# Optimization experiments

Measured on AMD Instinct MI355X. Metric: run time of the kernel, lower is better.

The kernel has to match this reference:

```python
import jax, jax.numpy as jnp
import numpy as np

T_TOK, N_UNITS, E, H, L_PATH, N_PATHS, B, VOCAB = 16, 4096, 128, 128, 32, 1024, 8, 16384
MAX_PATH_LEN = 32
PAD_ID = 0


def _run_lstm(x, Wi, Wh, b):
    # x: [T, N, E]; torch gate order i, f, g, o
    Hh = Wh.shape[1]
    h0 = jnp.zeros((x.shape[1], Hh), x.dtype)
    def step(carry, xt):
        h, c = carry
        g = xt @ Wi.T + h @ Wh.T + b
        i, f, gg, o = jnp.split(g, 4, axis=-1)
        c = jax.nn.sigmoid(f) * c + jax.nn.sigmoid(i) * jnp.tanh(gg)
        h = jax.nn.sigmoid(o) * jnp.tanh(c)
        return (h, c), h
    _, ys = jax.lax.scan(step, (h0, h0), x)
    return ys


def _bilstm(x, lengths, Wif, Whf, bf, Wib, Whb, bb):
    # emulates pack_padded_sequence + bidirectional LSTM + pad_packed (zeros past length)
    T = x.shape[0]
    t = jnp.arange(T)[:, None]
    valid = t < lengths[None, :]
    out_f = _run_lstm(x, Wif, Whf, bf)
    rev = jnp.clip(lengths[None, :] - 1 - t, 0, T - 1)  # reverse within each valid prefix
    x_rev = jnp.take_along_axis(x, rev[:, :, None], axis=0)
    out_b = jnp.take_along_axis(_run_lstm(x_rev, Wib, Whb, bb), rev[:, :, None], axis=0)
    return jnp.concatenate([out_f, out_b], axis=-1) * valid[:, :, None]


def _layernorm(x, g, b):
    m = x.mean(-1, keepdims=True)
    v = ((x - m) ** 2).mean(-1, keepdims=True)
    return (x - m) * jax.lax.rsqrt(v + 1e-5) * g + b


def _forward(units, paths, unit_per_data, path_per_data, emb, tl_Wif, tl_Whf, tl_bf,
             tl_Wib, tl_Whb, tl_bb, lin_W, lin_b, ln_g, ln_b, attn_w, attn_b,
             pl_Wif, pl_Whf, pl_bf, pl_Wib, pl_Whb, pl_bb, ul_W, ul_b):
    # ---- _token_encoder ----
    is_pad = units == PAD_ID
    tok_len = jnp.where(is_pad.any(0), jnp.argmax(is_pad, 0), units.shape[0])
    x = emb[units]                                              # [T, NU, E]
    h = _bilstm(x, tok_len, tl_Wif, tl_Whf, tl_bf, tl_Wib, tl_Whb, tl_bb)  # [T, NU, 2H]
    out = h @ lin_W.T + lin_b                                   # [T, NU, E]
    q = jnp.tanh(_layernorm(out, ln_g, ln_b))
    scores = q @ attn_w.T + attn_b                              # [T, NU, 1] local attention
    scores = jnp.where(is_pad[:, :, None], -1e9, scores)
    w = jax.nn.softmax(scores, axis=0)
    tok_feat = jnp.einsum('tn,tne->ne', w[..., 0], out)         # [NU, E]
    # ---- _unit_to_path (vectorized ragged gather) ----
    Lp, Pn = paths.shape
    has_end = (paths == -1).any(0)
    fe = jnp.where(has_end, jnp.argmax(paths == -1, 0), Lp)
    ML = min(Lp, MAX_PATH_LEN)
    nb = unit_per_data.shape[0]
    data_of_path = jnp.repeat(jnp.arange(nb), path_per_data, total_repeat_length=Pn)
    u_off = jnp.cumsum(unit_per_data) - unit_per_data
    off_p = u_off[data_of_path]
    un_p = unit_per_data[data_of_path]
    pL = paths[:ML]
    t = jnp.arange(ML)[:, None]
    within = t < fe[None, :]
    keep = within & (pL >= 0) & (pL < un_p[None, :])
    gidx = jnp.clip(jnp.clip(pL, 0, None) + off_p[None, :], 0, tok_feat.shape[0] - 1)
    feats = tok_feat[gidx] * keep[:, :, None]                   # [ML, P, E]
    mask = jnp.where(within, (pL < 0) | (pL > un_p[None, :]), True)
    # ---- _path_encoder ----
    p_len = jnp.where(mask.any(0), jnp.argmax(mask, 0), ML)
    hp = _bilstm(feats, p_len, pl_Wif, pl_Whf, pl_bf, pl_Wib, pl_Whb, pl_bb)
    return hp @ ul_W.T + ul_b                                   # [ML, P, E]


def setup_inputs() -> dict:
    rng = np.random.default_rng(0)
    tok_len = rng.integers(4, T_TOK + 1, N_UNITS); tok_len[0] = T_TOK
    units = rng.integers(1, VOCAB, (T_TOK, N_UNITS))
    units = np.where(np.arange(T_TOK)[:, None] < tok_len[None, :], units, PAD_ID)
    upd = N_UNITS // B
    p_len = rng.integers(8, L_PATH + 1, N_PATHS); p_len[0] = L_PATH
    paths = rng.integers(0, upd, (L_PATH, N_PATHS))
    paths = np.where(np.arange(L_PATH)[:, None] < p_len[None, :], paths, -1)
    key = jax.random.key(0)
    ks = iter(jax.random.split(key, 24))
    def pn(shape, s=0.08):
        return (jax.random.normal(next(ks), shape) * s).astype(jnp.float32)
    return dict(
        units=jnp.asarray(units, jnp.int32),
        paths=jnp.asarray(paths, jnp.int32),
        unit_per_data=jnp.full((B,), upd, jnp.int32),
        path_per_data=jnp.full((B,), N_PATHS // B, jnp.int32),
        emb=pn((VOCAB, E)),
        tl_Wif=pn((4 * H, E)), tl_Whf=pn((4 * H, H)), tl_bf=pn((4 * H,)),
        tl_Wib=pn((4 * H, E)), tl_Whb=pn((4 * H, H)), tl_bb=pn((4 * H,)),
        lin_W=pn((E, 2 * H)), lin_b=pn((E,)),
        ln_g=jnp.ones((E,), jnp.float32), ln_b=jnp.zeros((E,), jnp.float32),
        attn_w=pn((1, E)), attn_b=pn((1,)),
        pl_Wif=pn((4 * H, E)), pl_Whf=pn((4 * H, H)), pl_bf=pn((4 * H,)),
        pl_Wib=pn((4 * H, E)), pl_Whb=pn((4 * H, H)), pl_bb=pn((4 * H,)),
        ul_W=pn((E, 2 * H)), ul_b=pn((E,)),
    )


def reference(units, paths, unit_per_data, path_per_data, emb, tl_Wif, tl_Whf, tl_bf,
              tl_Wib, tl_Whb, tl_bb, lin_W, lin_b, ln_g, ln_b, attn_w, attn_b,
              pl_Wif, pl_Whf, pl_bf, pl_Wib, pl_Whb, pl_bb, ul_W, ul_b):
    return _forward(units, paths, unit_per_data, path_per_data, emb, tl_Wif, tl_Whf, tl_bf,
                    tl_Wib, tl_Whb, tl_bb, lin_W, lin_b, ln_g, ln_b, attn_w, attn_b,
                    pl_Wif, pl_Whf, pl_bf, pl_Wib, pl_Whb, pl_bb, ul_W, ul_b)
```

## Files before the change

### kernel.cpp

```cpp
#include <hip/hip_runtime.h>
#include <cstdint>
#include <cstddef>

#define T_TOKN 16
#define NUNITS 4096
#define LPATH  32
#define NPATHS 1024
#define BNUM   8

typedef __attribute__((ext_vector_type(8))) short short8;
typedef __attribute__((ext_vector_type(4))) short short4x;
typedef __attribute__((ext_vector_type(4))) float f32x4;

enum : size_t {
  OFF_WFRAG   = 0,
  OFF_LINFRAG = 262144,
  OFF_OUTF    = 294912,
  OFF_OUTB    = OFF_OUTF + 4194304,
  OFF_OUTLIN  = OFF_OUTB + 4194304,
  OFF_SCORES  = OFF_OUTLIN + 8388608,
  OFF_TOKFEAT = OFF_SCORES + 65536,
  OFF_POUTF   = OFF_TOKFEAT + 524288,
  OFF_POUTB   = OFF_POUTF + 2097152,
  OFF_INT     = OFF_POUTB + 2097152,
  WS_FLOATS   = OFF_INT + 8192
};

static __device__ __forceinline__ unsigned short f2bf(float f) {
  union { float f; unsigned u; } v; v.f = f;
  unsigned r = v.u + 0x7fffu + ((v.u >> 16) & 1u);
  return (unsigned short)(r >> 16);
}
static __device__ __forceinline__ float bf2f(unsigned short u) {
  union { unsigned u; float f; } v; v.u = ((unsigned)u) << 16;
  return v.f;
}
static __device__ __forceinline__ unsigned pack_bf(float a, float b) {
  return (unsigned)f2bf(a) | ((unsigned)f2bf(b) << 16);
}
static __device__ __forceinline__ float sigf(float x)      { return 1.f / (1.f + __expf(-x)); }
static __device__ __forceinline__ float tanhfast(float x)  { return 2.f / (1.f + __expf(-2.f * x)) - 1.f; }

__global__ void prep_kernel(
    const float* __restrict__ tWif, const float* __restrict__ tWhf,
    const float* __restrict__ tWib, const float* __restrict__ tWhb,
    const float* __restrict__ pWif, const float* __restrict__ pWhf,
    const float* __restrict__ pWib, const float* __restrict__ pWhb,
    const float* __restrict__ linW, const float* __restrict__ ulW,
    const int* __restrict__ units, const int* __restrict__ paths,
    const int* __restrict__ upd, const int* __restrict__ ppd,
    float* __restrict__ ws, int* __restrict__ ip)
{
  int idx = blockIdx.x * 256 + threadIdx.x;
  if (idx < 524288) {
    unsigned short* wf = (unsigned short*)(ws + OFF_WFRAG);
    int mat = idx >> 17, rem = idx & 131071;
    int i  = rem & 7;
    int lane = (rem >> 3) & 63;
    int ct = (rem >> 9) & 3;
    int ks = (rem >> 11) & 7;
    int wv = (rem >> 14) & 7;
    int g = wv * 64 + ct * 16 + (lane & 15);
    int k = ks * 32 + ((lane >> 4) << 3) + i;
    const float* Wi; const float* Wh;
    switch (mat) {
      case 0: Wi = tWif; Wh = tWhf; break;
      case 1: Wi = tWib; Wh = tWhb; break;
      case 2: Wi = pWif; Wh = pWhf; break;
      default: Wi = pWib; Wh = pWhb; break;
    }
    float v = (k < 128) ? Wi[g * 128 + k] : Wh[g * 128 + (k - 128)];
    wf[idx] = f2bf(v);
  } else if (idx < 524288 + 65536) {
    unsigned short* lf = (unsigned short*)(ws + OFF_LINFRAG);
    int i2 = idx - 524288;
    int mat = i2 >> 15, rem = i2 & 32767;
    int i  = rem & 7;
    int lane = (rem >> 3) & 63;
    int ks = (rem >> 9) & 7;
    int ct = (rem >> 12) & 7;
    int e = ct * 16 + (lane & 15);
    int k = ks * 32 + ((lane >> 4) << 3) + i;
    const float* W = mat ? ulW : linW;
    lf[i2] = f2bf(W[e * 256 + k]);
  } else if (idx < 589824 + 4096) {
    int n = idx - 589824;
    int len = T_TOKN;
    for (int t = 0; t < T_TOKN; ++t)
      if (units[t * NUNITS + n] == 0) { len = t; break; }
    ip[n] = len;
  } else if (idx < 589824 + 5120) {
    int p = idx - (589824 + 4096);
    int* fe_a  = ip + 4096;
    int* p_len = ip + 5120;
    int* off_p = ip + 6144;
    int* un_p  = ip + 7168;
    int cum = 0; int d = BNUM - 1;
    for (int dd = 0; dd < BNUM; ++dd) {
      int c2 = cum + ppd[dd];
      if (p < c2) { d = dd; break; }
      cum = c2;
    }
    int off = 0;
    for (int dd = 0; dd < d; ++dd) off += upd[dd];
    int un = upd[d];
    off_p[p] = off; un_p[p] = un;
    int f = LPATH;
    for (int t = 0; t < LPATH; ++t)
      if (paths[t * NPATHS + p] == -1) { f = t; break; }
    fe_a[p] = f;
    int pl = LPATH;
    for (int t = 0; t < LPATH; ++t) {
      int v = paths[t * NPATHS + p];
      if ((t >= f) || (v < 0) || (v > un)) { pl = t; break; }
    }
    p_len[p] = pl;
  }
}

template <int MODE>
__global__ __launch_bounds__(1024, 4) void lstm_kernel(
    const unsigned short* __restrict__ wfragAll,
    const float* __restrict__ biasF, const float* __restrict__ biasB,
    const float* __restrict__ src,
    const int* __restrict__ idxsrc,
    const int* __restrict__ lens,
    const int* __restrict__ fe_a, const int* __restrict__ off_p, const int* __restrict__ un_p,
    unsigned short* __restrict__ outF, unsigned short* __restrict__ outB)
{
  constexpr int NN   = MODE ? NPATHS : NUNITS;
  constexpr int TT   = MODE ? LPATH : T_TOKN;
  constexpr int M    = MODE ? 8 : 32;
  constexpr int MR   = MODE ? 16 : 32;
  constexpr int NRT  = MR / 16;
  constexpr int ASTR = 264;
  constexpr int GSTR = 514;

  __shared__ unsigned short ash[MR * ASTR];
  __shared__ float gates[MR * GSTR];
  __shared__ int   idxL[M * TT];

  int tid  = threadIdx.x;
  int dir  = blockIdx.y;
  int n0   = blockIdx.x * M;
  int lane = tid & 63, wv = tid >> 6;

  const unsigned short* wbase =
      wfragAll + (size_t)((MODE ? 2 : 0) + dir) * 131072;
  int wv8 = wv >> 1;
  short8 bfr[8][2];
#pragma unroll
  for (int ks = 0; ks < 8; ++ks)
#pragma unroll
    for (int c2 = 0; c2 < 2; ++c2) {
      int ct = ((wv & 1) << 1) | c2;
      bfr[ks][c2] = *(const short8*)&wbase[((((wv8 * 8 + ks) * 4 + ct) * 64) + lane) * 8];
    }

  if (MODE == 0) {
    for (int i = tid; i < MR * 128; i += 1024)
      ash[(i >> 7) * ASTR + 128 + (i & 127)] = 0;
  } else {
    for (int i = tid; i < MR * ASTR; i += 1024) ash[i] = 0;
  }
  for (int i = tid; i < M * TT; i += 1024) {
    int u = i / TT, tt = i - u * TT;
    idxL[i] = idxsrc[tt * NN + (n0 + u)];
  }

  const float* bcp = dir ? biasB : biasF;
  int j2 = MODE ? (tid & 127) : ((tid & 63) * 2);
  int ug = MODE ? (tid >> 7)  : (tid >> 6);
  float2 b2[4];
#pragma unroll
  for (int q = 0; q < 4; ++q) {
    if (MODE == 0) b2[q] = *(const float2*)&bcp[q * 128 + j2];
    else           b2[q] = make_float2(bcp[q * 128 + j2], 0.f);
  }
  constexpr int NU = MODE ? 1 : 2;
  float cst0[NU], cst1[NU];
  int   ulen[NU];
#pragma unroll
  for (int i = 0; i < NU; ++i) {
    cst0[i] = 0.f; cst1[i] = 0.f;
    ulen[i] = lens[n0 + ug * NU + i];
  }

  int gu, gk0;
  if (MODE == 0) { gu = tid >> 5; gk0 = (tid & 31) * 4; }
  else           { gu = tid >> 7; gk0 = tid & 127; }
  int gn = n0 + gu;
  int glen = lens[gn];
  int gfe = 0, goff = 0, gun = 0;
  if (MODE) { gfe = fe_a[gn]; goff = off_p[gn]; gun = un_p[gn]; }

  float4 xq; float xs;
  __syncthreads();

  {
    int tau = dir ? min(max(glen - 1, 0), TT - 1) : 0;
    int v = idxL[gu * TT + tau];
    if (MODE == 0) {
      xq = *(const float4*)&src[(size_t)v * 128 + gk0];
    } else {
      bool keep = (tau < gfe) && (v >= 0) && (v < gun);
      xs = keep ? src[(size_t)min(v + goff, NUNITS - 1) * 128 + gk0] : 0.f;
    }
  }
  if (MODE == 0) {
    short4x x4;
    x4[0] = (short)f2bf(xq.x); x4[1] = (short)f2bf(xq.y);
    x4[2] = (short)f2bf(xq.z); x4[3] = (short)f2bf(xq.w);
    *(short4x*)&ash[gu * ASTR + gk0] = x4;
  } else {
    ash[gu * ASTR + gk0] = f2bf(xs);
  }
  __syncthreads();

#pragma unroll 1
  for (int t = 0; t < TT; ++t) {
    {
      int tn = (t + 1 < TT) ? t + 1 : t;
      int taun = dir ? min(max(glen - 1 - tn, 0), TT - 1) : tn;
      int vn = idxL[gu * TT + taun];
      f32x4 acc[NRT][2];
#pragma unroll
      for (int rt = 0; rt < NRT; ++rt)
#pragma unroll
        for (int c2 = 0; c2 < 2; ++c2) {
          f32x4 z = {0.f, 0.f, 0.f, 0.f};
          acc[rt][c2] = z;
        }
#pragma unroll
      for (int ks = 0; ks < 8; ++ks) {
        short8 afr[NRT];
#pragma unroll
        for (int rt = 0; rt < NRT; ++rt)
          afr[rt] = *(const short8*)&ash[(rt * 16 + (lane & 15)) * ASTR + ks * 32 + ((lane >> 4) << 3)];
#pragma unroll
        for (int rt = 0; rt < NRT; ++rt)
#pragma unroll
          for (int c2 = 0; c2 < 2; ++c2)
            acc[rt][c2] = __builtin_amdgcn_mfma_f32_16x16x32_bf16(
                afr[rt], bfr[ks][c2], acc[rt][c2], 0, 0, 0);
      }
      if (MODE == 0) {
        xq = *(const float4*)&src[(size_t)vn * 128 + gk0];
      } else {
        bool keep = (taun < gfe) && (vn >= 0) && (vn < gun);
        xs = keep ? src[(size_t)min(vn + goff, NUNITS - 1) * 128 + gk0] : 0.f;
      }
#pragma unroll
      for (int rt = 0; rt < NRT; ++rt)
#pragma unroll
        for (int c2 = 0; c2 < 2; ++c2) {
          int g = wv * 32 + c2 * 16 + (lane & 15);
#pragma unroll
          for (int r = 0; r < 4; ++r) {
            int u = rt * 16 + ((lane >> 4) << 2) + r;
            gates[u * GSTR + g] = acc[rt][c2][r];
          }
        }
    }
    __syncthreads();

#pragma unroll
    for (int i = 0; i < NU; ++i) {
      int u = ug * NU + i;
      int n = n0 + u;
      int L = ulen[i];
      if (t < L) {
        if (MODE == 0) {
          float2 g0 = *(const float2*)&gates[u * GSTR + j2];
          float2 g1 = *(const float2*)&gates[u * GSTR + 128 + j2];
          float2 g2 = *(const float2*)&gates[u * GSTR + 256 + j2];
          float2 g3 = *(const float2*)&gates[u * GSTR + 384 + j2];
          float i0 = sigf(g0.x + b2[0].x), i1 = sigf(g0.y + b2[0].y);
          float f0 = sigf(g1.x + b2[1].x), f1 = sigf(g1.y + b2[1].y);
          float c0 = tanhfast(g2.x + b2[2].x), c1 = tanhfast(g2.y + b2[2].y);
          float o0 = sigf(g3.x + b2[3].x), o1 = sigf(g3.y + b2[3].y);
          float cA = f0 * cst0[i] + i0 * c0;
          float cB = f1 * cst1[i] + i1 * c1;
          cst0[i] = cA; cst1[i] = cB;
          unsigned hp = pack_bf(o0 * tanhfast(cA), o1 * tanhfast(cB));
          *(unsigned*)&ash[u * ASTR + 128 + j2] = hp;
          if (dir == 0) {
            *(unsigned*)&outF[((size_t)t * NN + n) * 128 + j2] = hp;
          } else {
            *(unsigned*)&outB[((size_t)(L - 1 - t) * NN + n) * 128 + j2] = hp;
          }
        } else {
          float p0 = gates[u * GSTR + j2]       + b2[0].x;
          float p1 = gates[u * GSTR + 128 + j2] + b2[1].x;
          float p2 = gates[u * GSTR + 256 + j2] + b2[2].x;
          float p3 = gates[u * GSTR + 384 + j2] + b2[3].x;
          float ig = sigf(p0), fg = sigf(p1), gg = tanhfast(p2), og = sigf(p3);
          float c = fg * cst0[i] + ig * gg;
          cst0[i] = c;
          unsigned short hb = f2bf(og * tanhfast(c));
          ash[u * ASTR + 128 + j2] = hb;
          if (dir == 0) outF[((size_t)t * NN + n) * 128 + j2] = hb;
          else          outB[((size_t)(L - 1 - t) * NN + n) * 128 + j2] = hb;
        }
      } else {
        if (MODE == 0) {
          if (dir == 0) *(unsigned*)&outF[((size_t)t * NN + n) * 128 + j2] = 0u;
          else          *(unsigned*)&outB[((size_t)t * NN + n) * 128 + j2] = 0u;
        } else {
          if (dir == 0) outF[((size_t)t * NN + n) * 128 + j2] = 0;
          else          outB[((size_t)t * NN + n) * 128 + j2] = 0;
        }
      }
    }
    if (t + 1 < TT) {
      if (MODE == 0) {
        short4x x4;
        x4[0] = (short)f2bf(xq.x); x4[1] = (short)f2bf(xq.y);
        x4[2] = (short)f2bf(xq.z); x4[3] = (short)f2bf(xq.w);
        *(short4x*)&ash[gu * ASTR + gk0] = x4;
      } else {
        ash[gu * ASTR + gk0] = f2bf(xs);
      }
    }
    __syncthreads();
  }
}

template <int EPI>
__global__ __launch_bounds__(256) void gemm_mfma(
    const unsigned short* __restrict__ INf, const unsigned short* __restrict__ INb,
    const int* __restrict__ lens,
    const unsigned short* __restrict__ Bfrag, const float* __restrict__ bias,
    void* __restrict__ OUTv, float* __restrict__ scores,
    const float* __restrict__ lng, const float* __restrict__ lnb,
    const float* __restrict__ attw, const float* __restrict__ attb,
    const int* __restrict__ units, int Nn)
{
  constexpr int OSTR = 132;
  __shared__ float outs[64 * OSTR];
  __shared__ float red1[256];
  __shared__ float red2[256];
  __shared__ float rowm[64], rowr[64];
  __shared__ float awsh[128], lgsh[128], lbsh[128];

  int tid = threadIdx.x, lane = tid & 63, wv = tid >> 6;
  int row0 = blockIdx.x * 64;
  int t = row0 / Nn, n0 = row0 % Nn;

  if (EPI == 1 && tid < 128) {
    awsh[tid] = attw[tid]; lgsh[tid] = lng[tid]; lbsh[tid] = lnb[tid];
  }

  short8 bfr[8][2];
#pragma unroll
  for (int ks = 0; ks < 8; ++ks)
#pragma unroll
    for (int c2 = 0; c2 < 2; ++c2) {
      int ct = wv * 2 + c2;
      bfr[ks][c2] = *(const short8*)&Bfrag[(((ct * 8 + ks) * 64) + lane) * 8];
    }

  int rb = lane & 15;
  int koq = (lane >> 4) << 3;
  bool val[4];
#pragma unroll
  for (int rt = 0; rt < 4; ++rt)
    val[rt] = (EPI == 1) ? true : (t < lens[n0 + rt * 16 + rb]);

  f32x4 acc[4][2];
#pragma unroll
  for (int rt = 0; rt < 4; ++rt)
#pragma unroll
    for (int c2 = 0; c2 < 2; ++c2) {
      f32x4 z = {0.f, 0.f, 0.f, 0.f};
      acc[rt][c2] = z;
    }

#pragma unroll
  for (int ks = 0; ks < 8; ++ks) {
    const unsigned short* P = (ks < 4) ? INf : INb;
    int koff = (ks & 3) * 32 + koq;
#pragma unroll
    for (int rt = 0; rt < 4; ++rt) {
      short8 a = {0, 0, 0, 0, 0, 0, 0, 0};
      if (val[rt])
        a = *(const short8*)&P[((size_t)(row0 + rt * 16 + rb)) * 128 + koff];
#pragma unroll
      for (int c2 = 0; c2 < 2; ++c2)
        acc[rt][c2] = __builtin_amdgcn_mfma_f32_16x16x32_bf16(
            a, bfr[ks][c2], acc[rt][c2], 0, 0, 0);
    }
  }

  float bc[2];
#pragma unroll
  for (int c2 = 0; c2 < 2; ++c2) bc[c2] = bias[wv * 32 + c2 * 16 + rb];
#pragma unroll
  for (int rt = 0; rt < 4; ++rt)
#pragma unroll
    for (int c2 = 0; c2 < 2; ++c2) {
      int col = wv * 32 + c2 * 16 + rb;
      int ub  = rt * 16 + ((lane >> 4) << 2);
#pragma unroll
      for (int r = 0; r < 4; ++r)
        outs[(ub + r) * OSTR + col] = acc[rt][c2][r] + bc[c2];
    }
  __syncthreads();

  int row = tid >> 2, seg = tid & 3;
  const float* rp = &outs[row * OSTR + seg * 32];
  size_t go = ((size_t)(row0 + row)) * 128 + seg * 32;

  if (EPI == 0) {
    float* OUT = (float*)OUTv;
#pragma unroll
    for (int x = 0; x < 8; ++x)
      *(f32x4*)&OUT[go + x * 4] = *(const f32x4*)&rp[x * 4];
  } else {
    unsigned short* OUT = (unsigned short*)OUTv;
    f32x4 v[8];
    float s = 0.f, s2 = 0.f;
#pragma unroll
    for (int x = 0; x < 8; ++x) {
      v[x] = *(const f32x4*)&rp[x * 4];
#pragma unroll
      for (int c = 0; c < 4; ++c) { s += v[x][c]; s2 += v[x][c] * v[x][c]; }
    }
    red1[tid] = s; red2[tid] = s2;
    __syncthreads();
    if (tid < 64) {
      float a = red1[tid * 4] + red1[tid * 4 + 1] + red1[tid * 4 + 2] + red1[tid * 4 + 3];
      float b = red2[tid * 4] + red2[tid * 4 + 1] + red2[tid * 4 + 2] + red2[tid * 4 + 3];
      float m = a * (1.f / 128.f);
      float var = b * (1.f / 128.f) - m * m;
      rowm[tid] = m;
      rowr[tid] = rsqrtf(var + 1e-5f);
    }
    __syncthreads();
    float m = rowm[row], rs = rowr[row];
    float sp = 0.f;
#pragma unroll
    for (int x = 0; x < 8; ++x) {
      short4x pv;
#pragma unroll
      for (int c = 0; c < 4; ++c) {
        int col = seg * 32 + x * 4 + c;
        float q = tanhfast((v[x][c] - m) * rs * lgsh[col] + lbsh[col]);
        sp += q * awsh[col];
        pv[c] = (short)f2bf(v[x][c]);
      }
      *(short4x*)&OUT[go + x * 4] = pv;
    }
    red1[tid] = sp;
    __syncthreads();
    if (tid < 64) {
      float s3 = red1[tid * 4] + red1[tid * 4 + 1] + red1[tid * 4 + 2] + red1[tid * 4 + 3]
               + attb[0];
      int n = n0 + tid;
      if (units[t * NUNITS + n] == 0) s3 = -1e9f;
      scores[t * NUNITS + n] = s3;
    }
  }
}

__global__ __launch_bounds__(128) void softmax_feat_kernel(
    const float* __restrict__ scores, const unsigned short* __restrict__ out_lin,
    float* __restrict__ tok_feat)
{
  int n = blockIdx.x;
  int e = threadIdx.x;
  float s[T_TOKN];
  float m = -1e30f;
#pragma unroll
  for (int t = 0; t < T_TOKN; ++t) { s[t] = scores[t * NUNITS + n]; m = fmaxf(m, s[t]); }
  float sum = 0.f;
#pragma unroll
  for (int t = 0; t < T_TOKN; ++t) { s[t] = expf(s[t] - m); sum += s[t]; }
  float inv = 1.f / sum;
  float a = 0.f;
#pragma unroll
  for (int t = 0; t < T_TOKN; ++t)
    a += s[t] * inv * bf2f(out_lin[((size_t)t * NUNITS + n) * 128 + e]);
  tok_feat[n * 128 + e] = a;
}

extern "C" void kernel_launch(void* const* d_in, const int* in_sizes, int n_in,
                              void* d_out, int out_size, void* d_ws, size_t ws_size,
                              hipStream_t stream)
{
  const int*   units = (const int*)d_in[0];
  const int*   paths = (const int*)d_in[1];
  const int*   upd   = (const int*)d_in[2];
  const int*   ppd   = (const int*)d_in[3];
  const float* emb   = (const float*)d_in[4];
  const float* tWif  = (const float*)d_in[5];
  const float* tWhf  = (const float*)d_in[6];
  const float* tbf   = (const float*)d_in[7];
  const float* tWib  = (const float*)d_in[8];
  const float* tWhb  = (const float*)d_in[9];
  const float* tbb   = (const float*)d_in[10];
  const float* linW  = (const float*)d_in[11];
  const float* linb  = (const float*)d_in[12];
  const float* lng   = (const float*)d_in[13];
  const float* lnb   = (const float*)d_in[14];
  const float* attw  = (const float*)d_in[15];
  const float* attb  = (const float*)d_in[16];
  const float* pWif  = (const float*)d_in[17];
  const float* pWhf  = (const float*)d_in[18];
  const float* pbf   = (const float*)d_in[19];
  const float* pWib  = (const float*)d_in[20];
  const float* pWhb  = (const float*)d_in[21];
  const float* pbb   = (const float*)d_in[22];
  const float* ulW   = (const float*)d_in[23];
  const float* ulb   = (const float*)d_in[24];

  float* ws = (float*)d_ws;
  int*   ip = (int*)(ws + OFF_INT);
  if (ws_size < WS_FLOATS * sizeof(float)) return;

  unsigned short* wfrag   = (unsigned short*)(ws + OFF_WFRAG);
  unsigned short* linfrag = (unsigned short*)(ws + OFF_LINFRAG);
  unsigned short* ulfrag  = linfrag + 32768;
  unsigned short* OUTF  = (unsigned short*)(ws + OFF_OUTF);
  unsigned short* OUTB  = (unsigned short*)(ws + OFF_OUTB);
  unsigned short* POUTF = (unsigned short*)(ws + OFF_POUTF);
  unsigned short* POUTB = (unsigned short*)(ws + OFF_POUTB);

  prep_kernel<<<2324, 256, 0, stream>>>(tWif, tWhf, tWib, tWhb,
                                        pWif, pWhf, pWib, pWhb,
                                        linW, ulW, units, paths, upd, ppd,
                                        ws, ip);

  lstm_kernel<0><<<dim3(128, 2), 1024, 0, stream>>>(
      wfrag, tbf, tbb, emb, units, ip , nullptr, nullptr, nullptr,
      OUTF, OUTB);

  gemm_mfma<1><<<1024, 256, 0, stream>>>(
      OUTF, OUTB, ip , linfrag, linb,
      (void*)(ws + OFF_OUTLIN), ws + OFF_SCORES, lng, lnb, attw, attb, units, NUNITS);

  softmax_feat_kernel<<<4096, 128, 0, stream>>>(
      ws + OFF_SCORES, (const unsigned short*)(ws + OFF_OUTLIN),
      ws + OFF_TOKFEAT);

  lstm_kernel<1><<<dim3(128, 2), 1024, 0, stream>>>(
      wfrag, pbf, pbb, ws + OFF_TOKFEAT, paths, ip + 5120 ,
      ip + 4096 , ip + 6144 , ip + 7168 ,
      POUTF, POUTB);

  gemm_mfma<0><<<512, 256, 0, stream>>>(
      POUTF, POUTB, ip + 5120 , ulfrag, ulb,
      (void*)d_out, nullptr, nullptr, nullptr, nullptr, nullptr, nullptr, NPATHS);
}
```

Measured before the change: 306.2 us.

## Vectorize weight-fragment prep and transpose LSTM gate buffer in shared memory

The prep kernel now has each thread read eight contiguous floats with float4 loads and write one short8 fragment, which cuts the thread count and launch size roughly eightfold. In the LSTM kernel the gate scratch buffer is transposed to gate-major with a padded unit stride. MFMA results are stored as float4 vectors, and each thread reads four units' gates for one hidden index with vector loads. This changes the per-thread work split (4 units × 1 column instead of 2 units × 2 columns) and alters the bank-conflict pattern. In exchange, hidden-state and output stores become 16-bit scalar writes instead of packed 32-bit writes.

```diff
diff --git a/kernel.cpp b/kernel.cpp
--- a/kernel.cpp
+++ b/kernel.cpp
@@ -35,9 +35,6 @@
   union { unsigned u; float f; } v; v.u = ((unsigned)u) << 16;
   return v.f;
 }
-static __device__ __forceinline__ unsigned pack_bf(float a, float b) {
-  return (unsigned)f2bf(a) | ((unsigned)f2bf(b) << 16);
-}
 static __device__ __forceinline__ float sigf(float x)      { return 1.f / (1.f + __expf(-x)); }
 static __device__ __forceinline__ float tanhfast(float x)  { return 2.f / (1.f + __expf(-2.f * x)) - 1.f; }
 
@@ -52,16 +49,9 @@
     float* __restrict__ ws, int* __restrict__ ip)
 {
   int idx = blockIdx.x * 256 + threadIdx.x;
-  if (idx < 524288) {
+  if (idx < 65536) {
     unsigned short* wf = (unsigned short*)(ws + OFF_WFRAG);
-    int mat = idx >> 17, rem = idx & 131071;
-    int i  = rem & 7;
-    int lane = (rem >> 3) & 63;
-    int ct = (rem >> 9) & 3;
-    int ks = (rem >> 11) & 7;
-    int wv = (rem >> 14) & 7;
-    int g = wv * 64 + ct * 16 + (lane & 15);
-    int k = ks * 32 + ((lane >> 4) << 3) + i;
+    int k8 = idx & 31, g = (idx >> 5) & 511, mat = idx >> 14;
     const float* Wi; const float* Wh;
     switch (mat) {
       case 0: Wi = tWif; Wh = tWhf; break;
@@ -69,28 +59,47 @@
       case 2: Wi = pWif; Wh = pWhf; break;
       default: Wi = pWib; Wh = pWhb; break;
     }
-    float v = (k < 128) ? Wi[g * 128 + k] : Wh[g * 128 + (k - 128)];
-    wf[idx] = f2bf(v);
-  } else if (idx < 524288 + 65536) {
+    int kb = k8 << 3;
+    const float* sp = (kb < 128) ? (Wi + g * 128 + kb) : (Wh + g * 128 + (kb - 128));
+    float4 a = *(const float4*)sp;
+    float4 b = *(const float4*)(sp + 4);
+    int wvp = g >> 6, ct = (g >> 4) & 3, cl = g & 15;
+    int ks = k8 >> 2, quad = k8 & 3;
+    size_t base = ((size_t)mat << 17) +
+                  (size_t)(((((wvp * 8 + ks) * 4 + ct) * 64) + quad * 16 + cl) << 3);
+    short8 o;
+    o[0] = (short)f2bf(a.x); o[1] = (short)f2bf(a.y);
+    o[2] = (short)f2bf(a.z); o[3] = (short)f2bf(a.w);
+    o[4] = (short)f2bf(b.x); o[5] = (short)f2bf(b.y);
+    o[6] = (short)f2bf(b.z); o[7] = (short)f2bf(b.w);
+    *(short8*)&wf[base] = o;
+  } else if (idx < 65536 + 8192) {
     unsigned short* lf = (unsigned short*)(ws + OFF_LINFRAG);
-    int i2 = idx - 524288;
-    int mat = i2 >> 15, rem = i2 & 32767;
-    int i  = rem & 7;
-    int lane = (rem >> 3) & 63;
-    int ks = (rem >> 9) & 7;
-    int ct = (rem >> 12) & 7;
-    int e = ct * 16 + (lane & 15);
-    int k = ks * 32 + ((lane >> 4) << 3) + i;
+    int j = idx - 65536;
+    int k8 = j & 31, e = (j >> 5) & 127, mat = j >> 12;
     const float* W = mat ? ulW : linW;
-    lf[i2] = f2bf(W[e * 256 + k]);
-  } else if (idx < 589824 + 4096) {
-    int n = idx - 589824;
+    int kb = k8 << 3;
+    const float* sp = W + e * 256 + kb;
+    float4 a = *(const float4*)sp;
+    float4 b = *(const float4*)(sp + 4);
+    int ct = e >> 4, cl = e & 15;
+    int ks = k8 >> 2, quad = k8 & 3;
+    size_t base = ((size_t)mat << 15) +
+                  (size_t)((((ct * 8 + ks) * 64) + quad * 16 + cl) << 3);
+    short8 o;
+    o[0] = (short)f2bf(a.x); o[1] = (short)f2bf(a.y);
+    o[2] = (short)f2bf(a.z); o[3] = (short)f2bf(a.w);
+    o[4] = (short)f2bf(b.x); o[5] = (short)f2bf(b.y);
+    o[6] = (short)f2bf(b.z); o[7] = (short)f2bf(b.w);
+    *(short8*)&lf[base] = o;
+  } else if (idx < 73728 + 4096) {
+    int n = idx - 73728;
     int len = T_TOKN;
     for (int t = 0; t < T_TOKN; ++t)
       if (units[t * NUNITS + n] == 0) { len = t; break; }
     ip[n] = len;
-  } else if (idx < 589824 + 5120) {
-    int p = idx - (589824 + 4096);
+  } else if (idx < 77824 + 1024) {
+    int p = idx - 77824;
     int* fe_a  = ip + 4096;
     int* p_len = ip + 5120;
     int* off_p = ip + 6144;
@@ -134,16 +143,17 @@
   constexpr int MR   = MODE ? 16 : 32;
   constexpr int NRT  = MR / 16;
   constexpr int ASTR = 264;
-  constexpr int GSTR = 514;
+  constexpr int USTR = MODE ? 17 : 36;
 
   __shared__ unsigned short ash[MR * ASTR];
-  __shared__ float gates[MR * GSTR];
+  __shared__ float gatesT[512 * USTR];
   __shared__ int   idxL[M * TT];
 
   int tid  = threadIdx.x;
   int dir  = blockIdx.y;
   int n0   = blockIdx.x * M;
   int lane = tid & 63, wv = tid >> 6;
+  int cl   = lane & 15, quad = lane >> 4;
 
   const unsigned short* wbase =
       wfragAll + (size_t)((MODE ? 2 : 0) + dir) * 131072;
@@ -169,20 +179,17 @@
   }
 
   const float* bcp = dir ? biasB : biasF;
-  int j2 = MODE ? (tid & 127) : ((tid & 63) * 2);
-  int ug = MODE ? (tid >> 7)  : (tid >> 6);
-  float2 b2[4];
-#pragma unroll
-  for (int q = 0; q < 4; ++q) {
-    if (MODE == 0) b2[q] = *(const float2*)&bcp[q * 128 + j2];
-    else           b2[q] = make_float2(bcp[q * 128 + j2], 0.f);
-  }
-  constexpr int NU = MODE ? 1 : 2;
-  float cst0[NU], cst1[NU];
+  const int jj  = tid & 127;
+  const int ug  = tid >> 7;
+  float bq[4];
+#pragma unroll
+  for (int q = 0; q < 4; ++q) bq[q] = bcp[q * 128 + jj];
+  constexpr int NU = MODE ? 1 : 4;
+  float cst[NU];
   int   ulen[NU];
 #pragma unroll
   for (int i = 0; i < NU; ++i) {
-    cst0[i] = 0.f; cst1[i] = 0.f;
+    cst[i] = 0.f;
     ulen[i] = lens[n0 + ug * NU + i];
   }
 
@@ -236,7 +243,7 @@
         short8 afr[NRT];
 #pragma unroll
         for (int rt = 0; rt < NRT; ++rt)
-          afr[rt] = *(const short8*)&ash[(rt * 16 + (lane & 15)) * ASTR + ks * 32 + ((lane >> 4) << 3)];
+          afr[rt] = *(const short8*)&ash[(rt * 16 + cl) * ASTR + ks * 32 + (quad << 3)];
 #pragma unroll
         for (int rt = 0; rt < NRT; ++rt)
 #pragma unroll
@@ -250,66 +257,67 @@
         bool keep = (taun < gfe) && (vn >= 0) && (vn < gun);
         xs = keep ? src[(size_t)min(vn + goff, NUNITS - 1) * 128 + gk0] : 0.f;
       }
-#pragma unroll
-      for (int rt = 0; rt < NRT; ++rt)
+      if constexpr (MODE == 0) {
+#pragma unroll
+        for (int rt = 0; rt < NRT; ++rt)
+#pragma unroll
+          for (int c2 = 0; c2 < 2; ++c2) {
+            int g = wv * 32 + c2 * 16 + cl;
+            *(f32x4*)&gatesT[g * USTR + rt * 16 + (quad << 2)] = acc[rt][c2];
+          }
+      } else {
 #pragma unroll
         for (int c2 = 0; c2 < 2; ++c2) {
-          int g = wv * 32 + c2 * 16 + (lane & 15);
-#pragma unroll
-          for (int r = 0; r < 4; ++r) {
-            int u = rt * 16 + ((lane >> 4) << 2) + r;
-            gates[u * GSTR + g] = acc[rt][c2][r];
-          }
+          int g = wv * 32 + c2 * 16 + cl;
+#pragma unroll
+          for (int r = 0; r < 4; ++r)
+            gatesT[g * USTR + (quad << 2) + r] = acc[0][c2][r];
         }
+      }
     }
     __syncthreads();
 
-#pragma unroll
-    for (int i = 0; i < NU; ++i) {
-      int u = ug * NU + i;
-      int n = n0 + u;
-      int L = ulen[i];
+    if constexpr (MODE == 0) {
+      f32x4 gq0 = *(const f32x4*)&gatesT[(0 * 128 + jj) * USTR + (ug << 2)];
+      f32x4 gq1 = *(const f32x4*)&gatesT[(1 * 128 + jj) * USTR + (ug << 2)];
+      f32x4 gq2 = *(const f32x4*)&gatesT[(2 * 128 + jj) * USTR + (ug << 2)];
+      f32x4 gq3 = *(const f32x4*)&gatesT[(3 * 128 + jj) * USTR + (ug << 2)];
+#pragma unroll
+      for (int r = 0; r < 4; ++r) {
+        int u = (ug << 2) + r, n = n0 + u, L = ulen[r];
+        if (t < L) {
+          float iv = sigf(gq0[r] + bq[0]);
+          float fv = sigf(gq1[r] + bq[1]);
+          float gv = tanhfast(gq2[r] + bq[2]);
+          float ov = sigf(gq3[r] + bq[3]);
+          float c = fv * cst[r] + iv * gv;
+          cst[r] = c;
+          unsigned short hb = f2bf(ov * tanhfast(c));
+          ash[u * ASTR + 128 + jj] = hb;
+          if (dir == 0) outF[((size_t)t * NN + n) * 128 + jj] = hb;
+          else          outB[((size_t)(L - 1 - t) * NN + n) * 128 + jj] = hb;
+        } else {
+          if (dir == 0) outF[((size_t)t * NN + n) * 128 + jj] = 0;
+          else          outB[((size_t)t * NN + n) * 128 + jj] = 0;
+        }
+      }
+    } else {
+      int u = ug, n = n0 + u, L = ulen[0];
       if (t < L) {
-        if (MODE == 0) {
-          float2 g0 = *(const float2*)&gates[u * GSTR + j2];
-          float2 g1 = *(const float2*)&gates[u * GSTR + 128 + j2];
-          float2 g2 = *(const float2*)&gates[u * GSTR + 256 + j2];
-          float2 g3 = *(const float2*)&gates[u * GSTR + 384 + j2];
-          float i0 = sigf(g0.x + b2[0].x), i1 = sigf(g0.y + b2[0].y);
-          float f0 = sigf(g1.x + b2[1].x), f1 = sigf(g1.y + b2[1].y);
-          float c0 = tanhfast(g2.x + b2[2].x), c1 = tanhfast(g2.y + b2[2].y);
-          float o0 = sigf(g3.x + b2[3].x), o1 = sigf(g3.y + b2[3].y);
-          float cA = f0 * cst0[i] + i0 * c0;
-          float cB = f1 * cst1[i] + i1 * c1;
-          cst0[i] = cA; cst1[i] = cB;
-          unsigned hp = pack_bf(o0 * tanhfast(cA), o1 * tanhfast(cB));
-          *(unsigned*)&ash[u * ASTR + 128 + j2] = hp;
-          if (dir == 0) {
-            *(unsigned*)&outF[((size_t)t * NN + n) * 128 + j2] = hp;
-          } else {
-            *(unsigned*)&outB[((size_t)(L - 1 - t) * NN + n) * 128 + j2] = hp;
-          }
-        } else {
-          float p0 = gates[u * GSTR + j2]       + b2[0].x;
-          float p1 = gates[u * GSTR + 128 + j2] + b2[1].x;
-          float p2 = gates[u * GSTR + 256 + j2] + b2[2].x;
-          float p3 = gates[u * GSTR + 384 + j2] + b2[3].x;
-          float ig = sigf(p0), fg = sigf(p1), gg = tanhfast(p2), og = sigf(p3);
-          float c = fg * cst0[i] + ig * gg;
-          cst0[i] = c;
-          unsigned short hb = f2bf(og * tanhfast(c));
-          ash[u * ASTR + 128 + j2] = hb;
-          if (dir == 0) outF[((size_t)t * NN + n) * 128 + j2] = hb;
-          else          outB[((size_t)(L - 1 - t) * NN + n) * 128 + j2] = hb;
-        }
+        float p0 = gatesT[(0 * 128 + jj) * USTR + u] + bq[0];
+        float p1 = gatesT[(1 * 128 + jj) * USTR + u] + bq[1];
+        float p2 = gatesT[(2 * 128 + jj) * USTR + u] + bq[2];
+        float p3 = gatesT[(3 * 128 + jj) * USTR + u] + bq[3];
+        float ig = sigf(p0), fg = sigf(p1), gg = tanhfast(p2), og = sigf(p3);
+        float c = fg * cst[0] + ig * gg;
+        cst[0] = c;
+        unsigned short hb = f2bf(og * tanhfast(c));
+        ash[u * ASTR + 128 + jj] = hb;
+        if (dir == 0) outF[((size_t)t * NN + n) * 128 + jj] = hb;
+        else          outB[((size_t)(L - 1 - t) * NN + n) * 128 + jj] = hb;
       } else {
-        if (MODE == 0) {
-          if (dir == 0) *(unsigned*)&outF[((size_t)t * NN + n) * 128 + j2] = 0u;
-          else          *(unsigned*)&outB[((size_t)t * NN + n) * 128 + j2] = 0u;
-        } else {
-          if (dir == 0) outF[((size_t)t * NN + n) * 128 + j2] = 0;
-          else          outB[((size_t)t * NN + n) * 128 + j2] = 0;
-        }
+        if (dir == 0) outF[((size_t)t * NN + n) * 128 + jj] = 0;
+        else          outB[((size_t)t * NN + n) * 128 + jj] = 0;
       }
     }
     if (t + 1 < TT) {
@@ -526,10 +534,10 @@
   unsigned short* POUTF = (unsigned short*)(ws + OFF_POUTF);
   unsigned short* POUTB = (unsigned short*)(ws + OFF_POUTB);
 
-  prep_kernel<<<2324, 256, 0, stream>>>(tWif, tWhf, tWib, tWhb,
-                                        pWif, pWhf, pWib, pWhb,
-                                        linW, ulW, units, paths, upd, ppd,
-                                        ws, ip);
+  prep_kernel<<<308, 256, 0, stream>>>(tWif, tWhf, tWib, tWhb,
+                                       pWif, pWhf, pWib, pWhb,
+                                       linW, ulW, units, paths, upd, ppd,
+                                       ws, ip);
 
   lstm_kernel<0><<<dim3(128, 2), 1024, 0, stream>>>(
       wfrag, tbf, tbb, emb, units, ip , nullptr, nullptr, nullptr,
```

Measured after the change: 307.6 us. About the same (+0.4%).

## Vectorize weight prep, store token features as bf16, skip padded output zeroing

Applied to the files above, without the earlier changes.

The prep kernel now gives each thread eight contiguous weights, read with float4 loads and written as one short8 fragment, so the grid shrinks from 2324 to 308 blocks. softmax_feat writes tok_feat in bf16, and the path LSTM reads it directly without converting, which halves that gather traffic. The LSTM no longer writes zeros for padded timesteps, and the GEMM always masks by length instead. This relies on the downstream masks to cover the positions left unwritten in the workspace.

```diff
diff --git a/kernel.cpp b/kernel.cpp
--- a/kernel.cpp
+++ b/kernel.cpp
@@ -52,16 +52,9 @@
     float* __restrict__ ws, int* __restrict__ ip)
 {
   int idx = blockIdx.x * 256 + threadIdx.x;
-  if (idx < 524288) {
+  if (idx < 65536) {
     unsigned short* wf = (unsigned short*)(ws + OFF_WFRAG);
-    int mat = idx >> 17, rem = idx & 131071;
-    int i  = rem & 7;
-    int lane = (rem >> 3) & 63;
-    int ct = (rem >> 9) & 3;
-    int ks = (rem >> 11) & 7;
-    int wv = (rem >> 14) & 7;
-    int g = wv * 64 + ct * 16 + (lane & 15);
-    int k = ks * 32 + ((lane >> 4) << 3) + i;
+    int k8 = idx & 31, g = (idx >> 5) & 511, mat = idx >> 14;
     const float* Wi; const float* Wh;
     switch (mat) {
       case 0: Wi = tWif; Wh = tWhf; break;
@@ -69,28 +62,47 @@
       case 2: Wi = pWif; Wh = pWhf; break;
       default: Wi = pWib; Wh = pWhb; break;
     }
-    float v = (k < 128) ? Wi[g * 128 + k] : Wh[g * 128 + (k - 128)];
-    wf[idx] = f2bf(v);
-  } else if (idx < 524288 + 65536) {
+    int kb = k8 << 3;
+    const float* sp = (kb < 128) ? (Wi + g * 128 + kb) : (Wh + g * 128 + (kb - 128));
+    float4 a = *(const float4*)sp;
+    float4 b = *(const float4*)(sp + 4);
+    int wvp = g >> 6, ct = (g >> 4) & 3, cl = g & 15;
+    int ks = k8 >> 2, quad = k8 & 3;
+    size_t base = ((size_t)mat << 17) +
+                  (size_t)(((((wvp * 8 + ks) * 4 + ct) * 64) + quad * 16 + cl) << 3);
+    short8 o;
+    o[0] = (short)f2bf(a.x); o[1] = (short)f2bf(a.y);
+    o[2] = (short)f2bf(a.z); o[3] = (short)f2bf(a.w);
+    o[4] = (short)f2bf(b.x); o[5] = (short)f2bf(b.y);
+    o[6] = (short)f2bf(b.z); o[7] = (short)f2bf(b.w);
+    *(short8*)&wf[base] = o;
+  } else if (idx < 65536 + 8192) {
     unsigned short* lf = (unsigned short*)(ws + OFF_LINFRAG);
-    int i2 = idx - 524288;
-    int mat = i2 >> 15, rem = i2 & 32767;
-    int i  = rem & 7;
-    int lane = (rem >> 3) & 63;
-    int ks = (rem >> 9) & 7;
-    int ct = (rem >> 12) & 7;
-    int e = ct * 16 + (lane & 15);
-    int k = ks * 32 + ((lane >> 4) << 3) + i;
+    int j = idx - 65536;
+    int k8 = j & 31, e = (j >> 5) & 127, mat = j >> 12;
     const float* W = mat ? ulW : linW;
-    lf[i2] = f2bf(W[e * 256 + k]);
-  } else if (idx < 589824 + 4096) {
-    int n = idx - 589824;
+    int kb = k8 << 3;
+    const float* sp = W + e * 256 + kb;
+    float4 a = *(const float4*)sp;
+    float4 b = *(const float4*)(sp + 4);
+    int ct = e >> 4, cl = e & 15;
+    int ks = k8 >> 2, quad = k8 & 3;
+    size_t base = ((size_t)mat << 15) +
+                  (size_t)((((ct * 8 + ks) * 64) + quad * 16 + cl) << 3);
+    short8 o;
+    o[0] = (short)f2bf(a.x); o[1] = (short)f2bf(a.y);
+    o[2] = (short)f2bf(a.z); o[3] = (short)f2bf(a.w);
+    o[4] = (short)f2bf(b.x); o[5] = (short)f2bf(b.y);
+    o[6] = (short)f2bf(b.z); o[7] = (short)f2bf(b.w);
+    *(short8*)&lf[base] = o;
+  } else if (idx < 73728 + 4096) {
+    int n = idx - 73728;
     int len = T_TOKN;
     for (int t = 0; t < T_TOKN; ++t)
       if (units[t * NUNITS + n] == 0) { len = t; break; }
     ip[n] = len;
-  } else if (idx < 589824 + 5120) {
-    int p = idx - (589824 + 4096);
+  } else if (idx < 77824 + 1024) {
+    int p = idx - 77824;
     int* fe_a  = ip + 4096;
     int* p_len = ip + 5120;
     int* off_p = ip + 6144;
@@ -122,7 +134,7 @@
 __global__ __launch_bounds__(1024, 4) void lstm_kernel(
     const unsigned short* __restrict__ wfragAll,
     const float* __restrict__ biasF, const float* __restrict__ biasB,
-    const float* __restrict__ src,
+    const void* __restrict__ srcv,
     const int* __restrict__ idxsrc,
     const int* __restrict__ lens,
     const int* __restrict__ fe_a, const int* __restrict__ off_p, const int* __restrict__ un_p,
@@ -140,6 +152,9 @@
   __shared__ float gates[MR * GSTR];
   __shared__ int   idxL[M * TT];
 
+  const float* srcf = (const float*)srcv;
+  const unsigned short* src16 = (const unsigned short*)srcv;
+
   int tid  = threadIdx.x;
   int dir  = blockIdx.y;
   int n0   = blockIdx.x * M;
@@ -194,17 +209,17 @@
   int gfe = 0, goff = 0, gun = 0;
   if (MODE) { gfe = fe_a[gn]; goff = off_p[gn]; gun = un_p[gn]; }
 
-  float4 xq; float xs;
+  float4 xq; unsigned short xs;
   __syncthreads();
 
   {
     int tau = dir ? min(max(glen - 1, 0), TT - 1) : 0;
     int v = idxL[gu * TT + tau];
     if (MODE == 0) {
-      xq = *(const float4*)&src[(size_t)v * 128 + gk0];
+      xq = *(const float4*)&srcf[(size_t)v * 128 + gk0];
     } else {
       bool keep = (tau < gfe) && (v >= 0) && (v < gun);
-      xs = keep ? src[(size_t)min(v + goff, NUNITS - 1) * 128 + gk0] : 0.f;
+      xs = keep ? src16[(size_t)min(v + goff, NUNITS - 1) * 128 + gk0] : (unsigned short)0;
     }
   }
   if (MODE == 0) {
@@ -213,7 +228,7 @@
     x4[2] = (short)f2bf(xq.z); x4[3] = (short)f2bf(xq.w);
     *(short4x*)&ash[gu * ASTR + gk0] = x4;
   } else {
-    ash[gu * ASTR + gk0] = f2bf(xs);
+    ash[gu * ASTR + gk0] = xs;
   }
   __syncthreads();
 
@@ -245,10 +260,10 @@
                 afr[rt], bfr[ks][c2], acc[rt][c2], 0, 0, 0);
       }
       if (MODE == 0) {
-        xq = *(const float4*)&src[(size_t)vn * 128 + gk0];
+        xq = *(const float4*)&srcf[(size_t)vn * 128 + gk0];
       } else {
         bool keep = (taun < gfe) && (vn >= 0) && (vn < gun);
-        xs = keep ? src[(size_t)min(vn + goff, NUNITS - 1) * 128 + gk0] : 0.f;
+        xs = keep ? src16[(size_t)min(vn + goff, NUNITS - 1) * 128 + gk0] : (unsigned short)0;
       }
 #pragma unroll
       for (int rt = 0; rt < NRT; ++rt)
@@ -284,11 +299,8 @@
           cst0[i] = cA; cst1[i] = cB;
           unsigned hp = pack_bf(o0 * tanhfast(cA), o1 * tanhfast(cB));
           *(unsigned*)&ash[u * ASTR + 128 + j2] = hp;
-          if (dir == 0) {
-            *(unsigned*)&outF[((size_t)t * NN + n) * 128 + j2] = hp;
-          } else {
-            *(unsigned*)&outB[((size_t)(L - 1 - t) * NN + n) * 128 + j2] = hp;
-          }
+          if (dir == 0) *(unsigned*)&outF[((size_t)t * NN + n) * 128 + j2] = hp;
+          else          *(unsigned*)&outB[((size_t)(L - 1 - t) * NN + n) * 128 + j2] = hp;
         } else {
           float p0 = gates[u * GSTR + j2]       + b2[0].x;
           float p1 = gates[u * GSTR + 128 + j2] + b2[1].x;
@@ -302,14 +314,6 @@
           if (dir == 0) outF[((size_t)t * NN + n) * 128 + j2] = hb;
           else          outB[((size_t)(L - 1 - t) * NN + n) * 128 + j2] = hb;
         }
-      } else {
-        if (MODE == 0) {
-          if (dir == 0) *(unsigned*)&outF[((size_t)t * NN + n) * 128 + j2] = 0u;
-          else          *(unsigned*)&outB[((size_t)t * NN + n) * 128 + j2] = 0u;
-        } else {
-          if (dir == 0) outF[((size_t)t * NN + n) * 128 + j2] = 0;
-          else          outB[((size_t)t * NN + n) * 128 + j2] = 0;
-        }
       }
     }
     if (t + 1 < TT) {
@@ -319,7 +323,7 @@
         x4[2] = (short)f2bf(xq.z); x4[3] = (short)f2bf(xq.w);
         *(short4x*)&ash[gu * ASTR + gk0] = x4;
       } else {
-        ash[gu * ASTR + gk0] = f2bf(xs);
+        ash[gu * ASTR + gk0] = xs;
       }
     }
     __syncthreads();
@@ -365,7 +369,7 @@
   bool val[4];
 #pragma unroll
   for (int rt = 0; rt < 4; ++rt)
-    val[rt] = (EPI == 1) ? true : (t < lens[n0 + rt * 16 + rb]);
+    val[rt] = (t < lens[n0 + rt * 16 + rb]);
 
   f32x4 acc[4][2];
 #pragma unroll
@@ -465,7 +469,7 @@
 
 __global__ __launch_bounds__(128) void softmax_feat_kernel(
     const float* __restrict__ scores, const unsigned short* __restrict__ out_lin,
-    float* __restrict__ tok_feat)
+    unsigned short* __restrict__ tok_feat)
 {
   int n = blockIdx.x;
   int e = threadIdx.x;
@@ -481,7 +485,7 @@
 #pragma unroll
   for (int t = 0; t < T_TOKN; ++t)
     a += s[t] * inv * bf2f(out_lin[((size_t)t * NUNITS + n) * 128 + e]);
-  tok_feat[n * 128 + e] = a;
+  tok_feat[n * 128 + e] = f2bf(a);
 }
 
 extern "C" void kernel_launch(void* const* d_in, const int* in_sizes, int n_in,
@@ -525,26 +529,26 @@
   unsigned short* OUTB  = (unsigned short*)(ws + OFF_OUTB);
   unsigned short* POUTF = (unsigned short*)(ws + OFF_POUTF);
   unsigned short* POUTB = (unsigned short*)(ws + OFF_POUTB);
-
-  prep_kernel<<<2324, 256, 0, stream>>>(tWif, tWhf, tWib, tWhb,
-                                        pWif, pWhf, pWib, pWhb,
-                                        linW, ulW, units, paths, upd, ppd,
-                                        ws, ip);
+  unsigned short* TOKF16 = (unsigned short*)(ws + OFF_TOKFEAT);
+
+  prep_kernel<<<308, 256, 0, stream>>>(tWif, tWhf, tWib, tWhb,
+                                       pWif, pWhf, pWib, pWhb,
+                                       linW, ulW, units, paths, upd, ppd,
+                                       ws, ip);
 
   lstm_kernel<0><<<dim3(128, 2), 1024, 0, stream>>>(
-      wfrag, tbf, tbb, emb, units, ip , nullptr, nullptr, nullptr,
-      OUTF, OUTB);
+      wfrag, tbf, tbb, (const void*)emb, units, ip ,
+      nullptr, nullptr, nullptr, OUTF, OUTB);
 
   gemm_mfma<1><<<1024, 256, 0, stream>>>(
       OUTF, OUTB, ip , linfrag, linb,
       (void*)(ws + OFF_OUTLIN), ws + OFF_SCORES, lng, lnb, attw, attb, units, NUNITS);
 
   softmax_feat_kernel<<<4096, 128, 0, stream>>>(
-      ws + OFF_SCORES, (const unsigned short*)(ws + OFF_OUTLIN),
-      ws + OFF_TOKFEAT);
+      ws + OFF_SCORES, (const unsigned short*)(ws + OFF_OUTLIN), TOKF16);
 
   lstm_kernel<1><<<dim3(128, 2), 1024, 0, stream>>>(
-      wfrag, pbf, pbb, ws + OFF_TOKFEAT, paths, ip + 5120 ,
+      wfrag, pbf, pbb, (const void*)TOKF16, paths, ip + 5120 ,
       ip + 4096 , ip + 6144 , ip + 7168 ,
       POUTF, POUTB);
 
```

Result: no change. 303.3 us (-0.9%).
